# Optimization experiments

Hardware: AMD Instinct MI355X
Metric: run time of the kernel (lower is better)

Reference implementation:

```python
import jax, jax.numpy as jnp
import numpy as np

B, H, M, K = 256, 1024, 20, 20  # batch, hidden, max_ingr, pairing top_k (must be equal: M==K)
VOCAB, INGR_V = 32000, 5000


def setup_inputs() -> dict:
    key = jax.random.key(0)
    ks = jax.random.split(key, 24)
    s = 0.02
    inp = {
        "input_ids": jax.random.randint(ks[0], (1, B), 0, VOCAB),
        "hidden": jax.random.normal(ks[1], (1, B, H), jnp.float32),
        "encoder_outputs": jax.random.normal(ks[2], (M, B, 2 * H), jnp.float32),
        "input_tensor": jax.random.randint(ks[3], (B, M), 0, INGR_V),
        "pairing_ids": jax.random.randint(ks[4], (INGR_V, K), 0, INGR_V),
        # parameters
        "emb_dec": jax.random.normal(ks[5], (VOCAB, H), jnp.float32) * s,
        "enc_emb": jax.random.normal(ks[6], (INGR_V, 2 * H), jnp.float32) * s,
        "Wq_i": jax.random.normal(ks[7], (H, H), jnp.float32) * s,
        "Wk_i": jax.random.normal(ks[8], (2 * H, H), jnp.float32) * s,
        "wa_i": jax.random.normal(ks[9], (H,), jnp.float32) * s,
        "Wq_p": jax.random.normal(ks[10], (H, H), jnp.float32) * s,
        "Wk_p": jax.random.normal(ks[11], (2 * H, H), jnp.float32) * s,
        "wa_p": jax.random.normal(ks[12], (H,), jnp.float32) * s,
        "ba_p": jax.random.normal(ks[13], (), jnp.float32) * s,
        "W_lin": jax.random.normal(ks[14], (3 * H, 2 * H), jnp.float32) * s,
        "b_lin": jnp.zeros((2 * H,), jnp.float32),
        "W_ih": jax.random.normal(ks[15], (3 * H, 2 * H), jnp.float32) * s,
        "W_hh": jax.random.normal(ks[16], (3 * H, H), jnp.float32) * s,
        "b_ih": jnp.zeros((3 * H,), jnp.float32),
        "b_hh": jnp.zeros((3 * H,), jnp.float32),
        "W_out": jax.random.normal(ks[17], (H, VOCAB), jnp.float32) * s,
        "b_out": jnp.zeros((VOCAB,), jnp.float32),
    }
    return inp


def reference(input_ids, hidden, encoder_outputs, input_tensor, pairing_ids,
              emb_dec, enc_emb, Wq_i, Wk_i, wa_i, Wq_p, Wk_p, wa_p, ba_p,
              W_lin, b_lin, W_ih, W_hh, b_ih, b_hh, W_out, b_out):
    h = hidden[0]                              # (B, H)
    emb = jnp.take(emb_dec, input_ids[0], axis=0)  # (B, H)

    # ---- IngrAtt (additive attention over ingredients) ----
    # torch code does a raw .view(B, M, 2H) on a (M, B, 2H) tensor -> plain reshape
    enc = encoder_outputs.reshape(B, M, 2 * H)
    query = h @ Wq_i                           # (B, H)
    key = enc @ Wk_i                           # (B, M, H)
    scores_i = jnp.tanh(query[:, None, :] + key) @ wa_i  # (B, M)
    aw = jax.nn.softmax(scores_i, axis=-1)     # (B, M)

    # ---- retrieval: pick most-attended ingredient, gather its top-k pairings ----
    ingr_arg = jnp.argmax(aw, axis=1)                          # (B,)
    ingr_id = input_tensor[jnp.arange(B), ingr_arg]            # (B,)
    comp_ids = jnp.take(pairing_ids, ingr_id, axis=0)          # (B, K)
    comp_emb = jnp.take(enc_emb, comp_ids, axis=0)             # (B, K, 2H)

    # ---- PairingAtt ----
    q_p = h @ Wq_p                             # (B, H)
    k_p = comp_emb @ Wk_p                      # (B, K, H)
    s_p = jnp.tanh(q_p[:, None, :] + k_p) @ wa_p + ba_p  # (B, K)
    a_p = jax.nn.softmax(s_p, axis=-1)
    attn_scores = a_p * s_p                    # (B, K) softmax-weighted raw scores
    attn_app = jnp.einsum('bk,bkd->bd', attn_scores, comp_emb)  # (B, 2H)

    out_pair = jnp.concatenate([emb, attn_app], axis=-1)  # (B, 3H)
    x = out_pair @ W_lin + b_lin                           # (B, 2H) -> GRU input

    # ---- single GRU step (torch gate ordering r,z,n) ----
    gi = x @ W_ih.T + b_ih
    gh = h @ W_hh.T + b_hh
    i_r, i_z, i_n = jnp.split(gi, 3, axis=-1)
    h_r, h_z, h_n = jnp.split(gh, 3, axis=-1)
    r = jax.nn.sigmoid(i_r + h_r)
    z = jax.nn.sigmoid(i_z + h_z)
    n = jnp.tanh(i_n + r * h_n)
    h_new = (1.0 - z) * n + z * h              # (B, H)

    logits = h_new @ W_out + b_out             # (B, VOCAB)
    return logits
```

## Files before the change

### kernel.cpp

```cpp
#include <hip/hip_runtime.h>
#include <cstdio>


using f32x4   = __attribute__((ext_vector_type(4))) float;
using bf16x8  = __attribute__((ext_vector_type(8))) short;
using ushort8 = __attribute__((ext_vector_type(8))) unsigned short;

__device__ __forceinline__ unsigned short f2bf(float x) {
    unsigned u = __builtin_bit_cast(unsigned, x);
    u += 0x7fffu + ((u >> 16) & 1u);
    return (unsigned short)(u >> 16);
}
__device__ __forceinline__ float bf2f(unsigned short u) {
    return __builtin_bit_cast(float, ((unsigned)u) << 16);
}

__device__ __forceinline__ void gload16(const void* g, void* l) {
    auto gp = (const __attribute__((address_space(1))) void*)g;
    auto lp = (__attribute__((address_space(3))) void*)l;
    __builtin_amdgcn_global_load_lds(gp, lp, 16, 0, 0);
}

__device__ __forceinline__ void transpose_body(
    const float* __restrict__ in, unsigned short* __restrict__ out,
    int R, int C, int r0, int c0)
{
    __shared__ float t[32][129];
    const int tid = threadIdx.x;
    const int lr = tid >> 3;
    const int cc = (tid & 7) * 4;
    #pragma unroll
    for (int i = 0; i < 4; ++i) {
        int r = lr + 32 * i;
        float4 v = *(const float4*)(in + (size_t)(r0 + r) * C + c0 + cc);
        t[cc + 0][r] = v.x; t[cc + 1][r] = v.y;
        t[cc + 2][r] = v.z; t[cc + 3][r] = v.w;
    }
    __syncthreads();
    const int rc = (tid & 15) * 8;
    #pragma unroll
    for (int p = 0; p < 2; ++p) {
        int c = (tid >> 4) + 16 * p;
        const float* src = &t[c][rc];
        ushort8 o;
        #pragma unroll
        for (int j = 0; j < 8; ++j) o[j] = f2bf(src[j]);
        *(ushort8*)(out + (size_t)(c0 + c) * R + r0 + rc) = o;
    }
}

__global__ __launch_bounds__(256) void prep1_kernel(
    const float* __restrict__ hidden, const float* __restrict__ enc_out,
    const float* __restrict__ enc_emb,
    const float* __restrict__ Wq_i, const float* __restrict__ Wq_p,
    const float* __restrict__ Wk_i, const float* __restrict__ Wk_p,
    unsigned short* __restrict__ hb, unsigned short* __restrict__ encb,
    unsigned short* __restrict__ encembb,
    unsigned short* __restrict__ WqiT, unsigned short* __restrict__ WqpT,
    unsigned short* __restrict__ WkiT, unsigned short* __restrict__ WkpT)
{
    const int bid = blockIdx.x;
    if (bid < 20496) {
        int i = bid * 256 + threadIdx.x;
        const float* src; unsigned short* dst; int j;
        if (i < 65536)        { src = hidden;  dst = hb;      j = i; }
        else if (i < 2686976) { src = enc_out; dst = encb;    j = i - 65536; }
        else                  { src = enc_emb; dst = encembb; j = i - 2686976; }
        float4 v = ((const float4*)src)[j];
        ((ushort4*)dst)[j] = make_ushort4(f2bf(v.x), f2bf(v.y), f2bf(v.z), f2bf(v.w));
    } else if (bid < 21008) {
        int local = bid - 20496;
        int bz = local >> 8, rem = local & 255;
        transpose_body(bz ? Wq_p : Wq_i, bz ? WqpT : WqiT,
                       1024, 1024, (rem >> 5) * 128, (rem & 31) * 32);
    } else {
        int local = bid - 21008;
        int bz = local >> 9, rem = local & 511;
        transpose_body(bz ? Wk_p : Wk_i, bz ? WkpT : WkiT,
                       2048, 1024, (rem >> 5) * 128, (rem & 31) * 32);
    }
}

__global__ __launch_bounds__(256) void transpose1_kernel(
    const float* in, unsigned short* out, int R, int C)
{ transpose_body(in, out, R, C, blockIdx.y * 128, blockIdx.x * 32); }

__global__ __launch_bounds__(256) void conv2w_kernel(
    const float* __restrict__ Wih, const float* __restrict__ Whh,
    unsigned short* __restrict__ ob0, unsigned short* __restrict__ ob1)
{
    int i = blockIdx.x * 256 + threadIdx.x;
    const float* src; unsigned short* dst; int j;
    if (i < 1572864) { src = Wih; dst = ob0; j = i; }
    else             { src = Whh; dst = ob1; j = i - 1572864; }
    float4 v = ((const float4*)src)[j];
    ((ushort4*)dst)[j] = make_ushort4(f2bf(v.x), f2bf(v.y), f2bf(v.z), f2bf(v.w));
}

template<int OUTBF, bool HAS_BIAS>
__device__ __forceinline__ void gemm_core(
    const unsigned short* __restrict__ A, const unsigned short* __restrict__ Bt,
    const float* __restrict__ bias, void* __restrict__ Cout, int Ncols,
    int sA, int sB, int kLen, int m0, int n0,
    unsigned short* lA, unsigned short* lB)
{
    const int tid = threadIdx.x;
    const int lane = tid & 63, wave = tid >> 6;
    const int wr = wave >> 1, wc = wave & 1;
    const int srow = tid >> 3, schunk = tid & 7;
    const int lm = lane & 15, lk = (lane >> 4) * 8;

    f32x4 acc[4][4];
    #pragma unroll
    for (int m = 0; m < 4; ++m)
        #pragma unroll
        for (int n = 0; n < 4; ++n) { f32x4 z = {0.f,0.f,0.f,0.f}; acc[m][n] = z; }

    const unsigned short* Ag = A  + (size_t)(m0 + srow) * sA + schunk * 8;
    const unsigned short* Bg = Bt + (size_t)(n0 + srow) * sB + schunk * 8;
    const int nt = kLen >> 6;

    char* lap = (char*)lA + tid * 16;
    char* lbp = (char*)lB + tid * 16;

    for (int t = 0; t < nt; ++t) {
        #pragma unroll
        for (int i = 0; i < 4; ++i) {
            gload16(Ag + (size_t)(32 * i) * sA + t * 64, lap + i * 4096);
            gload16(Bg + (size_t)(32 * i) * sB + t * 64, lbp + i * 4096);
        }
        __syncthreads();
        #pragma unroll
        for (int kk = 0; kk < 2; ++kk) {
            bf16x8 af[4], bv[4];
            #pragma unroll
            for (int m = 0; m < 4; ++m)
                af[m] = *(const bf16x8*)((const char*)lA +
                          (wr * 64 + m * 16 + lm) * 128 + (kk * 32 + lk) * 2);
            #pragma unroll
            for (int n = 0; n < 4; ++n)
                bv[n] = *(const bf16x8*)((const char*)lB +
                          (wc * 64 + n * 16 + lm) * 128 + (kk * 32 + lk) * 2);
            #pragma unroll
            for (int m = 0; m < 4; ++m)
                #pragma unroll
                for (int n = 0; n < 4; ++n)
                    acc[m][n] = __builtin_amdgcn_mfma_f32_16x16x32_bf16(
                        af[m], bv[n], acc[m][n], 0, 0, 0);
        }
        __syncthreads();
    }

    const int rbase = m0 + wr * 64 + (lane >> 4) * 4;
    const int cbase = n0 + wc * 64 + lm;
    #pragma unroll
    for (int m = 0; m < 4; ++m) {
        #pragma unroll
        for (int n = 0; n < 4; ++n) {
            int col = cbase + n * 16;
            float bvv = HAS_BIAS ? bias[col] : 0.0f;
            #pragma unroll
            for (int j = 0; j < 4; ++j) {
                int row = rbase + m * 16 + j;
                float v = acc[m][n][j] + bvv;
                if (OUTBF)
                    ((unsigned short*)Cout)[(size_t)row * Ncols + col] = f2bf(v);
                else
                    ((float*)Cout)[(size_t)row * Ncols + col] = v;
            }
        }
    }
}

#define GEMM_SHARED \
    __shared__ unsigned short lA[8192]; __shared__ unsigned short lB[8192];

__global__ __launch_bounds__(256) void gemm_dual_kernel(
    const unsigned short* A, const unsigned short* B0, const unsigned short* B1,
    float* P0, float* P1)
{
    GEMM_SHARED
    const int g = blockIdx.z >> 2, s = blockIdx.z & 3;
    const unsigned short* Bt = (g ? B1 : B0) + s * 256;
    float* C = (g ? P1 : P0) + (size_t)s * 262144;
    gemm_core<0,false>(A + s * 256, Bt, nullptr, C, 1024, 1024, 1024, 256,
                       blockIdx.y * 128, blockIdx.x * 128, lA, lB);
}

__global__ __launch_bounds__(256) void reduceq_kernel(
    const float* __restrict__ pqQ, const float* __restrict__ pqP,
    float* __restrict__ query, float* __restrict__ qp)
{
    int i = blockIdx.x * 256 + threadIdx.x;
    const float4* p; float4* o; int j;
    if (i < 65536) { p = (const float4*)pqQ; o = (float4*)query; j = i; }
    else           { p = (const float4*)pqP; o = (float4*)qp;    j = i - 65536; }
    float4 a = p[j], b = p[j + 65536], c = p[j + 131072], d = p[j + 196608];
    o[j] = make_float4(a.x + b.x + c.x + d.x, a.y + b.y + c.y + d.y,
                       a.z + b.z + c.z + d.z, a.w + b.w + c.w + d.w);
}

__global__ __launch_bounds__(256) void gemm24_kernel(
    const unsigned short* encembb, const unsigned short* encb,
    const unsigned short* WkpT, const unsigned short* WkiT,
    unsigned short* kp_all, unsigned short* key)
{
    GEMM_SHARED
    const int z = blockIdx.z;
    const unsigned short* A  = z ? encb : encembb;
    const unsigned short* Bt = z ? WkiT : WkpT;
    unsigned short* C = z ? key : kp_all;
    gemm_core<1,false>(A, Bt, nullptr, C, 1024, 2048, 2048, 2048,
                       blockIdx.y * 128, blockIdx.x * 128, lA, lB);
}

__global__ __launch_bounds__(256) void gemm5_kernel(
    const unsigned short* A, const unsigned short* Bt, float* P)
{
    GEMM_SHARED
    const int z = blockIdx.z;
    gemm_core<0,false>(A + z * 384, Bt + z * 384, nullptr,
                       P + (size_t)z * 524288, 2048, 3072, 3072, 384,
                       blockIdx.y * 128, blockIdx.x * 128, lA, lB);
}

__global__ __launch_bounds__(256) void gemm67_kernel(
    const unsigned short* xb, const unsigned short* hb,
    const unsigned short* Wih, const unsigned short* Whh, float* pg)
{
    GEMM_SHARED
    const int g = blockIdx.z >> 2, s = blockIdx.z & 3;
    const unsigned short* A  = g ? hb  + s * 256 : xb  + s * 512;
    const unsigned short* Bt = g ? Whh + s * 256 : Wih + s * 512;
    const int sAB  = g ? 1024 : 2048;
    const int kLen = g ? 256  : 512;
    float* C = pg + (size_t)blockIdx.z * 786432;
    gemm_core<0,false>(A, Bt, nullptr, C, 3072, sAB, sAB, kLen,
                       blockIdx.y * 128, blockIdx.x * 128, lA, lB);
}

__global__ __launch_bounds__(256) void gemm8_kernel(
    const unsigned short* __restrict__ A, const float* __restrict__ Wout,
    const float* __restrict__ bias, float* __restrict__ C)
{
    __shared__ unsigned short lA0[16384]; __shared__ unsigned short lA1[16384];
    __shared__ unsigned short lB0[4096];  __shared__ unsigned short lB1[4096];
    const int tid  = threadIdx.x;
    const int lane = tid & 63, wave = tid >> 6;
    const int n0 = blockIdx.x * 64;
    const int lm = lane & 15, lk = (lane >> 4) * 8;
    const int srow = tid >> 3, schunk = tid & 7;
    const int bcol = tid & 63, bkg = tid >> 6;
    const int bsw  = (bcol & 7) << 4;

    f32x4 acc[4][4];
    #pragma unroll
    for (int m = 0; m < 4; ++m)
        #pragma unroll
        for (int n = 0; n < 4; ++n) { f32x4 z = {0.f,0.f,0.f,0.f}; acc[m][n] = z; }

    const unsigned short* Ag = A + (size_t)srow * 1024 + schunk * 8;

    auto stageA = [&](unsigned short* la_, int t) {
        char* la = (char*)la_ + tid * 16;
        #pragma unroll
        for (int i = 0; i < 8; ++i)
            gload16(Ag + (size_t)(32 * i) * 1024 + t * 64, la + i * 4096);
    };
    float bv_[16];
    auto loadB = [&](int t) {
        const float* src = Wout + (size_t)(t * 64 + bkg * 16) * 32000 + n0 + bcol;
        #pragma unroll
        for (int j = 0; j < 16; ++j) bv_[j] = src[(size_t)j * 32000];
    };
    auto writeB = [&](unsigned short* lb_) {
        ushort8 o0, o1;
        #pragma unroll
        for (int j = 0; j < 8; ++j) { o0[j] = f2bf(bv_[j]); o1[j] = f2bf(bv_[j + 8]); }
        char* base = (char*)lb_ + bcol * 128;
        *(ushort8*)(base + ((bkg * 32)      ^ bsw)) = o0;
        *(ushort8*)(base + ((bkg * 32 + 16) ^ bsw)) = o1;
    };
    auto compute = [&](const unsigned short* la_, const unsigned short* lb_) {
        #pragma unroll
        for (int kk = 0; kk < 2; ++kk) {
            bf16x8 af[4], bv[4];
            #pragma unroll
            for (int m = 0; m < 4; ++m)
                af[m] = *(const bf16x8*)((const char*)la_ +
                          (wave * 64 + m * 16 + lm) * 128 + (kk * 32 + lk) * 2);
            #pragma unroll
            for (int n = 0; n < 4; ++n) {
                int rr = n * 16 + lm;
                bv[n] = *(const bf16x8*)((const char*)lb_ +
                          rr * 128 + (((kk * 32 + lk) * 2) ^ ((rr & 7) << 4)));
            }
            #pragma unroll
            for (int m = 0; m < 4; ++m)
                #pragma unroll
                for (int n = 0; n < 4; ++n)
                    acc[m][n] = __builtin_amdgcn_mfma_f32_16x16x32_bf16(
                        af[m], bv[n], acc[m][n], 0, 0, 0);
        }
    };

    stageA(lA0, 0); loadB(0); writeB(lB0);
    __syncthreads();
    const int nt = 16;
    for (int t = 0; t < nt; t += 2) {
        if (t + 1 < nt) { stageA(lA1, t + 1); loadB(t + 1); }
        compute(lA0, lB0);
        if (t + 1 < nt) writeB(lB1);
        __syncthreads();
        if (t + 1 < nt) {
            if (t + 2 < nt) { stageA(lA0, t + 2); loadB(t + 2); }
            compute(lA1, lB1);
            if (t + 2 < nt) writeB(lB0);
            __syncthreads();
        }
    }

    const int rbase = wave * 64 + (lane >> 4) * 4;
    const int cbase = n0 + lm;
    #pragma unroll
    for (int m = 0; m < 4; ++m) {
        #pragma unroll
        for (int n = 0; n < 4; ++n) {
            int col = cbase + n * 16;
            float bvv = bias[col];
            #pragma unroll
            for (int j = 0; j < 4; ++j)
                C[(size_t)(rbase + m * 16 + j) * 32000 + col] = acc[m][n][j] + bvv;
        }
    }
}

__global__ __launch_bounds__(256) void attn_scores_kernel(
    const float* __restrict__ q, const unsigned short* __restrict__ k,
    const float* __restrict__ wa, float* __restrict__ scores)
{
    const int bm = blockIdx.x;
    const int b  = bm / 20;
    const int tid = threadIdx.x;
    float4 qv  = ((const float4*)(q + (size_t)b * 1024))[tid];
    ushort4 kv = ((const ushort4*)(k + (size_t)bm * 1024))[tid];
    float4 wv  = ((const float4*)wa)[tid];
    float p = tanhf(qv.x + bf2f(kv.x)) * wv.x + tanhf(qv.y + bf2f(kv.y)) * wv.y
            + tanhf(qv.z + bf2f(kv.z)) * wv.z + tanhf(qv.w + bf2f(kv.w)) * wv.w;
    #pragma unroll
    for (int off = 32; off > 0; off >>= 1) p += __shfl_down(p, off);
    __shared__ float sp[4];
    if ((tid & 63) == 0) sp[tid >> 6] = p;
    __syncthreads();
    if (tid == 0) scores[bm] = sp[0] + sp[1] + sp[2] + sp[3];
}

__device__ __forceinline__ int argmax_ing(
    const float* __restrict__ sc_i, const int* __restrict__ input_tensor, int b)
{
    float best = sc_i[b * 20]; int bi = 0;
    #pragma unroll
    for (int m = 1; m < 20; ++m) {
        float v = sc_i[b * 20 + m];
        if (v > best) { best = v; bi = m; }
    }
    return input_tensor[b * 20 + bi];
}

__global__ __launch_bounds__(256) void attn_scores_gather_kernel(
    const float* __restrict__ q, const unsigned short* __restrict__ kp_all,
    const float* __restrict__ wa, const float* __restrict__ ba,
    const float* __restrict__ sc_i, const int* __restrict__ input_tensor,
    const int* __restrict__ pairing_ids, float* __restrict__ scores)
{
    const int bm = blockIdx.x;
    const int b  = bm / 20;
    const int kk = bm - b * 20;
    const int tid = threadIdx.x;
    const int ing = argmax_ing(sc_i, input_tensor, b);
    const int cid = pairing_ids[ing * 20 + kk];
    float4 qv  = ((const float4*)(q + (size_t)b * 1024))[tid];
    ushort4 kv = ((const ushort4*)(kp_all + (size_t)cid * 1024))[tid];
    float4 wv  = ((const float4*)wa)[tid];
    float p = tanhf(qv.x + bf2f(kv.x)) * wv.x + tanhf(qv.y + bf2f(kv.y)) * wv.y
            + tanhf(qv.z + bf2f(kv.z)) * wv.z + tanhf(qv.w + bf2f(kv.w)) * wv.w;
    #pragma unroll
    for (int off = 32; off > 0; off >>= 1) p += __shfl_down(p, off);
    __shared__ float sp[4];
    if ((tid & 63) == 0) sp[tid >> 6] = p;
    __syncthreads();
    if (tid == 0) scores[bm] = sp[0] + sp[1] + sp[2] + sp[3] + ba[0];
}

__global__ __launch_bounds__(256) void out_pair_kernel(
    const float* __restrict__ s_p, const float* __restrict__ enc_emb,
    const float* __restrict__ sc_i, const int* __restrict__ input_tensor,
    const int* __restrict__ pairing_ids,
    const float* __restrict__ emb_dec, const int* __restrict__ input_ids,
    unsigned short* __restrict__ out_pairb)
{
    const int b = blockIdx.x / 6, seg = blockIdx.x % 6;
    const int tid = threadIdx.x;
    const int d = seg * 512 + tid * 2;
    ushort2 o;
    if (seg < 2) {
        float2 v = *(const float2*)(emb_dec + (size_t)input_ids[b] * 1024 + d);
        o.x = f2bf(v.x); o.y = f2bf(v.y);
    } else {
        const int ing = argmax_ing(sc_i, input_tensor, b);
        __shared__ float s_raw[20];
        if (tid < 20) s_raw[tid] = s_p[b * 20 + tid];
        __syncthreads();
        float mx = -1e30f;
        #pragma unroll
        for (int m = 0; m < 20; ++m) mx = fmaxf(mx, s_raw[m]);
        float den = 0.f; float w[20];
        #pragma unroll
        for (int m = 0; m < 20; ++m) { w[m] = expf(s_raw[m] - mx); den += w[m]; }
        const float inv = 1.f / den;
        const int dd = d - 1024;
        float a0 = 0.f, a1 = 0.f;
        #pragma unroll
        for (int k = 0; k < 20; ++k) {
            const int cid = pairing_ids[ing * 20 + k];
            float2 v = *(const float2*)(enc_emb + (size_t)cid * 2048 + dd);
            float a = w[k] * inv * s_raw[k];
            a0 += a * v.x; a1 += a * v.y;
        }
        o.x = f2bf(a0); o.y = f2bf(a1);
    }
    *(ushort2*)(out_pairb + (size_t)b * 3072 + d) = o;
}

__global__ __launch_bounds__(256) void reduce5_kernel(
    const float* __restrict__ P, const float* __restrict__ bias,
    unsigned short* __restrict__ xb)
{
    int i = blockIdx.x * 256 + threadIdx.x;
    const float4* p = (const float4*)P;
    float4 bb = ((const float4*)bias)[i & 511];
    float s0 = bb.x, s1 = bb.y, s2 = bb.z, s3 = bb.w;
    #pragma unroll
    for (int s = 0; s < 8; ++s) {
        float4 v = p[i + s * 131072];
        s0 += v.x; s1 += v.y; s2 += v.z; s3 += v.w;
    }
    ((ushort4*)xb)[i] = make_ushort4(f2bf(s0), f2bf(s1), f2bf(s2), f2bf(s3));
}

__global__ __launch_bounds__(256) void gru_kernel(
    const float* __restrict__ pg, const float* __restrict__ b_ih,
    const float* __restrict__ b_hh, const float* __restrict__ h,
    unsigned short* __restrict__ hnewb)
{
    int idx = blockIdx.x * 256 + threadIdx.x;
    int b = idx >> 10, j = idx & 1023;
    float ir = b_ih[j], iz = b_ih[1024 + j], in_ = b_ih[2048 + j];
    float hr = b_hh[j], hz = b_hh[1024 + j], hn  = b_hh[2048 + j];
    #pragma unroll
    for (int s = 0; s < 4; ++s) {
        const float* gi = pg + (size_t)s * 786432 + (size_t)b * 3072;
        ir  += gi[j]; iz += gi[1024 + j]; in_ += gi[2048 + j];
        const float* gh = pg + (size_t)(4 + s) * 786432 + (size_t)b * 3072;
        hr  += gh[j]; hz += gh[1024 + j]; hn  += gh[2048 + j];
    }
    float r = 1.f / (1.f + expf(-(ir + hr)));
    float z = 1.f / (1.f + expf(-(iz + hz)));
    float n = tanhf(in_ + r * hn);
    hnewb[idx] = f2bf((1.f - z) * n + z * h[idx]);
}

extern "C" void kernel_launch(void* const* d_in, const int* in_sizes, int n_in,
                              void* d_out, int out_size, void* d_ws, size_t ws_size,
                              hipStream_t stream)
{
    const int*   input_ids    = (const int*)  d_in[0];
    const float* hidden       = (const float*)d_in[1];
    const float* enc_out      = (const float*)d_in[2];
    const int*   input_tensor = (const int*)  d_in[3];
    const int*   pairing_ids  = (const int*)  d_in[4];
    const float* emb_dec      = (const float*)d_in[5];
    const float* enc_emb      = (const float*)d_in[6];
    const float* Wq_i  = (const float*)d_in[7];
    const float* Wk_i  = (const float*)d_in[8];
    const float* wa_i  = (const float*)d_in[9];
    const float* Wq_p  = (const float*)d_in[10];
    const float* Wk_p  = (const float*)d_in[11];
    const float* wa_p  = (const float*)d_in[12];
    const float* ba_p  = (const float*)d_in[13];
    const float* W_lin = (const float*)d_in[14];
    const float* b_lin = (const float*)d_in[15];
    const float* W_ih  = (const float*)d_in[16];
    const float* W_hh  = (const float*)d_in[17];
    const float* b_ih  = (const float*)d_in[18];
    const float* b_hh  = (const float*)d_in[19];
    const float* W_out = (const float*)d_in[20];
    const float* b_out = (const float*)d_in[21];

    constexpr size_t OFF_HB    = 0;
    constexpr size_t OFF_HNEW  = 524288;
    constexpr size_t OFF_WQI   = 1048576;
    constexpr size_t OFF_WQP   = 3145728;
    constexpr size_t OFF_WKI   = 5242880;
    constexpr size_t OFF_WKP   = 9437184;
    constexpr size_t OFF_ENC   = 13631488;
    constexpr size_t OFF_SLOT1 = 34603008;
    constexpr size_t OFF_SLOT2 = 55574528;
    constexpr size_t OFF_QUERY = 76546048;
    constexpr size_t OFF_QP    = 77594624;
    constexpr size_t OFF_SCI   = 78643200;
    constexpr size_t OFF_SCP   = 78667776;
    constexpr size_t OFF_PGI   = 1048576;
    constexpr size_t NEED      = 79167488;
    if (ws_size < NEED) {
        fprintf(stderr, "kernel_launch: ws_size %zu < needed %zu\n", ws_size, NEED);
        return;
    }
    char* ws = (char*)d_ws;
    unsigned short* hb     = (unsigned short*)(ws + OFF_HB);
    unsigned short* hnewb  = (unsigned short*)(ws + OFF_HNEW);
    unsigned short* WqiT   = (unsigned short*)(ws + OFF_WQI);
    unsigned short* WqpT   = (unsigned short*)(ws + OFF_WQP);
    unsigned short* WkiT   = (unsigned short*)(ws + OFF_WKI);
    unsigned short* WkpT   = (unsigned short*)(ws + OFF_WKP);
    unsigned short* encb   = (unsigned short*)(ws + OFF_ENC);
    float*          pqQ    = (float*)         (ws + OFF_SLOT1);
    float*          pqP    = (float*)         (ws + OFF_SLOT1 + 4194304);
    unsigned short* kp_all = (unsigned short*)(ws + OFF_SLOT1);
    unsigned short* key    = (unsigned short*)(ws + OFF_SLOT1 + 10485760);
    unsigned short* encembb= (unsigned short*)(ws + OFF_SLOT2);
    unsigned short* WlinT  = (unsigned short*)(ws + OFF_SLOT2);
    unsigned short* Wihb   = (unsigned short*)(ws + OFF_SLOT2);
    unsigned short* Whhb   = (unsigned short*)(ws + OFF_SLOT2 + 12582912);
    unsigned short* outp   = (unsigned short*)(ws + OFF_SLOT1);
    float*          pG5    = (float*)         (ws + OFF_SLOT1 + 1572864);
    unsigned short* xb     = (unsigned short*)(ws + OFF_SLOT1 + 18350080);
    float*          query  = (float*)         (ws + OFF_QUERY);
    float*          qp     = (float*)         (ws + OFF_QP);
    float*          sc_i   = (float*)         (ws + OFF_SCI);
    float*          sc_p   = (float*)         (ws + OFF_SCP);
    float*          pgi    = (float*)         (ws + OFF_PGI);

    prep1_kernel<<<22032, 256, 0, stream>>>(hidden, enc_out, enc_emb,
                                            Wq_i, Wq_p, Wk_i, Wk_p,
                                            hb, encb, encembb,
                                            WqiT, WqpT, WkiT, WkpT);

    gemm_dual_kernel<<<dim3(8, 2, 8), 256, 0, stream>>>(hb, WqiT, WqpT, pqQ, pqP);
    reduceq_kernel<<<512, 256, 0, stream>>>(pqQ, pqP, query, qp);

    gemm24_kernel<<<dim3(8, 40, 2), 256, 0, stream>>>(encembb, encb, WkpT, WkiT,
                                                      kp_all, key);

    attn_scores_kernel<<<5120, 256, 0, stream>>>(query, key, wa_i, sc_i);
    attn_scores_gather_kernel<<<5120, 256, 0, stream>>>(qp, kp_all, wa_p, ba_p,
                                                        sc_i, input_tensor, pairing_ids, sc_p);

    out_pair_kernel<<<1536, 256, 0, stream>>>(sc_p, enc_emb, sc_i, input_tensor,
                                              pairing_ids, emb_dec, input_ids, outp);

    transpose1_kernel<<<dim3(64, 24), 256, 0, stream>>>(W_lin, WlinT, 3072, 2048);
    gemm5_kernel<<<dim3(16, 2, 8), 256, 0, stream>>>(outp, WlinT, pG5);
    reduce5_kernel<<<512, 256, 0, stream>>>(pG5, b_lin, xb);

    conv2w_kernel<<<9216, 256, 0, stream>>>(W_ih, W_hh, Wihb, Whhb);
    gemm67_kernel<<<dim3(24, 2, 8), 256, 0, stream>>>(xb, hb, Wihb, Whhb, pgi);

    gru_kernel<<<1024, 256, 0, stream>>>(pgi, b_ih, b_hh, hidden, hnewb);

    gemm8_kernel<<<500, 256, 0, stream>>>(hnewb, W_out, b_out, (float*)d_out);
}
```

Before: 241.2 us.

## Fuse fp32-to-bf16 weight conversion into GEMMs and split-K the key projections

The standalone W_lin transpose and the W_ih/W_hh bf16 conversion kernels are removed. The GEMM kernels now read fp32 weights directly and convert them to bf16 while staging into LDS, which saves a full write and reread of the converted weights. Separately, the key-projection GEMM is split along K into two halves that store bf16 partials (one set placed in the output buffer as scratch). The attention score kernels sum the two partials. This adds launch parallelism but doubles the key reads, adds an extra bf16 rounding, and turns the W_lin B loads into strided scalar reads.

Result: faster. 230.6 us (-4.4%).

```diff
diff --git a/kernel.cpp b/kernel.cpp
--- a/kernel.cpp
+++ b/kernel.cpp
@@ -81,22 +81,6 @@
     }
 }
 
-__global__ __launch_bounds__(256) void transpose1_kernel(
-    const float* in, unsigned short* out, int R, int C)
-{ transpose_body(in, out, R, C, blockIdx.y * 128, blockIdx.x * 32); }
-
-__global__ __launch_bounds__(256) void conv2w_kernel(
-    const float* __restrict__ Wih, const float* __restrict__ Whh,
-    unsigned short* __restrict__ ob0, unsigned short* __restrict__ ob1)
-{
-    int i = blockIdx.x * 256 + threadIdx.x;
-    const float* src; unsigned short* dst; int j;
-    if (i < 1572864) { src = Wih; dst = ob0; j = i; }
-    else             { src = Whh; dst = ob1; j = i - 1572864; }
-    float4 v = ((const float4*)src)[j];
-    ((ushort4*)dst)[j] = make_ushort4(f2bf(v.x), f2bf(v.y), f2bf(v.z), f2bf(v.w));
-}
-
 template<int OUTBF, bool HAS_BIAS>
 __device__ __forceinline__ void gemm_core(
     const unsigned short* __restrict__ A, const unsigned short* __restrict__ Bt,
@@ -203,40 +187,175 @@
 __global__ __launch_bounds__(256) void gemm24_kernel(
     const unsigned short* encembb, const unsigned short* encb,
     const unsigned short* WkpT, const unsigned short* WkiT,
-    unsigned short* kp_all, unsigned short* key)
+    unsigned short* kpP, unsigned short* keyP, size_t pStride)
 {
     GEMM_SHARED
-    const int z = blockIdx.z;
-    const unsigned short* A  = z ? encb : encembb;
-    const unsigned short* Bt = z ? WkiT : WkpT;
-    unsigned short* C = z ? key : kp_all;
-    gemm_core<1,false>(A, Bt, nullptr, C, 1024, 2048, 2048, 2048,
+    const int g = blockIdx.z >> 1, h = blockIdx.z & 1;
+    const unsigned short* A  = (g ? encb : encembb) + h * 1024;
+    const unsigned short* Bt = (g ? WkiT : WkpT)    + h * 1024;
+    unsigned short* C = (g ? keyP : kpP) + (size_t)h * pStride;
+    gemm_core<1,false>(A, Bt, nullptr, C, 1024, 2048, 2048, 1024,
                        blockIdx.y * 128, blockIdx.x * 128, lA, lB);
 }
 
-__global__ __launch_bounds__(256) void gemm5_kernel(
-    const unsigned short* A, const unsigned short* Bt, float* P)
-{
-    GEMM_SHARED
-    const int z = blockIdx.z;
-    gemm_core<0,false>(A + z * 384, Bt + z * 384, nullptr,
-                       P + (size_t)z * 524288, 2048, 3072, 3072, 384,
-                       blockIdx.y * 128, blockIdx.x * 128, lA, lB);
-}
-
-__global__ __launch_bounds__(256) void gemm67_kernel(
-    const unsigned short* xb, const unsigned short* hb,
-    const unsigned short* Wih, const unsigned short* Whh, float* pg)
-{
-    GEMM_SHARED
+__global__ __launch_bounds__(256) void gemm5f_kernel(
+    const unsigned short* __restrict__ A, const float* __restrict__ Wlin,
+    float* __restrict__ P)
+{
+    __shared__ unsigned short lA[8192];
+    __shared__ unsigned short lB[8192];
+    const int tid = threadIdx.x;
+    const int lane = tid & 63, wave = tid >> 6;
+    const int wr = wave >> 1, wc = wave & 1;
+    const int m0 = blockIdx.y * 128, n0 = blockIdx.x * 128;
+    const int koff = blockIdx.z * 384;
+    const int srow = tid >> 3, schunk = tid & 7;
+    const int lm = lane & 15, lk = (lane >> 4) * 8;
+    const int bcol = tid & 127, bkg = tid >> 7;
+    const int bsw  = (bcol & 7) << 4;
+
+    f32x4 acc[4][4];
+    #pragma unroll
+    for (int m = 0; m < 4; ++m)
+        #pragma unroll
+        for (int n = 0; n < 4; ++n) { f32x4 z = {0.f,0.f,0.f,0.f}; acc[m][n] = z; }
+
+    const unsigned short* Ag = A + (size_t)(m0 + srow) * 3072 + koff + schunk * 8;
+    char* lap = (char*)lA + tid * 16;
+
+    for (int t = 0; t < 6; ++t) {
+        #pragma unroll
+        for (int i = 0; i < 4; ++i)
+            gload16(Ag + (size_t)(32 * i) * 3072 + t * 64, lap + i * 4096);
+        #pragma unroll
+        for (int hh = 0; hh < 2; ++hh) {
+            const int kbase = koff + t * 64 + bkg * 32 + hh * 16;
+            ushort8 o0, o1;
+            #pragma unroll
+            for (int j = 0; j < 8; ++j)
+                o0[j] = f2bf(Wlin[(size_t)(kbase + j) * 2048 + n0 + bcol]);
+            #pragma unroll
+            for (int j = 0; j < 8; ++j)
+                o1[j] = f2bf(Wlin[(size_t)(kbase + 8 + j) * 2048 + n0 + bcol]);
+            char* base = (char*)lB + bcol * 128;
+            *(ushort8*)(base + ((bkg * 64 + hh * 32)      ^ bsw)) = o0;
+            *(ushort8*)(base + ((bkg * 64 + hh * 32 + 16) ^ bsw)) = o1;
+        }
+        __syncthreads();
+        #pragma unroll
+        for (int kk = 0; kk < 2; ++kk) {
+            bf16x8 af[4], bv[4];
+            #pragma unroll
+            for (int m = 0; m < 4; ++m)
+                af[m] = *(const bf16x8*)((const char*)lA +
+                          (wr * 64 + m * 16 + lm) * 128 + (kk * 32 + lk) * 2);
+            #pragma unroll
+            for (int n = 0; n < 4; ++n) {
+                int rr = wc * 64 + n * 16 + lm;
+                bv[n] = *(const bf16x8*)((const char*)lB +
+                          rr * 128 + (((kk * 32 + lk) * 2) ^ ((rr & 7) << 4)));
+            }
+            #pragma unroll
+            for (int m = 0; m < 4; ++m)
+                #pragma unroll
+                for (int n = 0; n < 4; ++n)
+                    acc[m][n] = __builtin_amdgcn_mfma_f32_16x16x32_bf16(
+                        af[m], bv[n], acc[m][n], 0, 0, 0);
+        }
+        __syncthreads();
+    }
+
+    float* C = P + (size_t)blockIdx.z * 524288;
+    const int rbase = m0 + wr * 64 + (lane >> 4) * 4;
+    const int cbase = n0 + wc * 64 + lm;
+    #pragma unroll
+    for (int m = 0; m < 4; ++m)
+        #pragma unroll
+        for (int n = 0; n < 4; ++n)
+            #pragma unroll
+            for (int j = 0; j < 4; ++j)
+                C[(size_t)(rbase + m * 16 + j) * 2048 + cbase + n * 16] = acc[m][n][j];
+}
+
+__global__ __launch_bounds__(256) void gemm67f_kernel(
+    const unsigned short* __restrict__ xb, const unsigned short* __restrict__ hb,
+    const float* __restrict__ Wih, const float* __restrict__ Whh,
+    float* __restrict__ pg)
+{
+    __shared__ unsigned short lA[8192];
+    __shared__ unsigned short lB[8192];
+    const int tid = threadIdx.x;
+    const int lane = tid & 63, wave = tid >> 6;
+    const int wr = wave >> 1, wc = wave & 1;
     const int g = blockIdx.z >> 2, s = blockIdx.z & 3;
-    const unsigned short* A  = g ? hb  + s * 256 : xb  + s * 512;
-    const unsigned short* Bt = g ? Whh + s * 256 : Wih + s * 512;
-    const int sAB  = g ? 1024 : 2048;
-    const int kLen = g ? 256  : 512;
+    const unsigned short* A = g ? hb : xb;
+    const float* Bf = g ? Whh : Wih;
+    const int sA   = g ? 1024 : 2048;
+    const int koff = g ? s * 256 : s * 512;
+    const int nt   = g ? 4 : 8;
+    const int m0 = blockIdx.y * 128, n0 = blockIdx.x * 128;
+    const int srow = tid >> 3, schunk = tid & 7;
+    const int lm = lane & 15, lk = (lane >> 4) * 8;
+    const int bsw = (srow & 7) << 4;
+
+    f32x4 acc[4][4];
+    #pragma unroll
+    for (int m = 0; m < 4; ++m)
+        #pragma unroll
+        for (int n = 0; n < 4; ++n) { f32x4 z = {0.f,0.f,0.f,0.f}; acc[m][n] = z; }
+
+    const unsigned short* Ag = A  + (size_t)(m0 + srow) * sA + koff + schunk * 8;
+    const float*          Bg = Bf + (size_t)(n0 + srow) * sA + koff + schunk * 8;
+    char* lap = (char*)lA + tid * 16;
+
+    for (int t = 0; t < nt; ++t) {
+        #pragma unroll
+        for (int i = 0; i < 4; ++i)
+            gload16(Ag + (size_t)(32 * i) * sA + t * 64, lap + i * 4096);
+        #pragma unroll
+        for (int i = 0; i < 4; ++i) {
+            const float* src = Bg + (size_t)(32 * i) * sA + t * 64;
+            float4 v0 = *(const float4*)(src);
+            float4 v1 = *(const float4*)(src + 4);
+            ushort8 o;
+            o[0] = f2bf(v0.x); o[1] = f2bf(v0.y); o[2] = f2bf(v0.z); o[3] = f2bf(v0.w);
+            o[4] = f2bf(v1.x); o[5] = f2bf(v1.y); o[6] = f2bf(v1.z); o[7] = f2bf(v1.w);
+            *(ushort8*)((char*)lB + (srow + 32 * i) * 128 + ((schunk * 16) ^ bsw)) = o;
+        }
+        __syncthreads();
+        #pragma unroll
+        for (int kk = 0; kk < 2; ++kk) {
+            bf16x8 af[4], bv[4];
+            #pragma unroll
+            for (int m = 0; m < 4; ++m)
+                af[m] = *(const bf16x8*)((const char*)lA +
+                          (wr * 64 + m * 16 + lm) * 128 + (kk * 32 + lk) * 2);
+            #pragma unroll
+            for (int n = 0; n < 4; ++n) {
+                int rr = wc * 64 + n * 16 + lm;
+                bv[n] = *(const bf16x8*)((const char*)lB +
+                          rr * 128 + (((kk * 32 + lk) * 2) ^ ((rr & 7) << 4)));
+            }
+            #pragma unroll
+            for (int m = 0; m < 4; ++m)
+                #pragma unroll
+                for (int n = 0; n < 4; ++n)
+                    acc[m][n] = __builtin_amdgcn_mfma_f32_16x16x32_bf16(
+                        af[m], bv[n], acc[m][n], 0, 0, 0);
+        }
+        __syncthreads();
+    }
+
     float* C = pg + (size_t)blockIdx.z * 786432;
-    gemm_core<0,false>(A, Bt, nullptr, C, 3072, sAB, sAB, kLen,
-                       blockIdx.y * 128, blockIdx.x * 128, lA, lB);
+    const int rbase = m0 + wr * 64 + (lane >> 4) * 4;
+    const int cbase = n0 + wc * 64 + lm;
+    #pragma unroll
+    for (int m = 0; m < 4; ++m)
+        #pragma unroll
+        for (int n = 0; n < 4; ++n)
+            #pragma unroll
+            for (int j = 0; j < 4; ++j)
+                C[(size_t)(rbase + m * 16 + j) * 3072 + cbase + n * 16] = acc[m][n][j];
 }
 
 __global__ __launch_bounds__(256) void gemm8_kernel(
@@ -335,18 +454,21 @@
     }
 }
 
-__global__ __launch_bounds__(256) void attn_scores_kernel(
-    const float* __restrict__ q, const unsigned short* __restrict__ k,
-    const float* __restrict__ wa, float* __restrict__ scores)
+__global__ __launch_bounds__(256) void attn_scores2_kernel(
+    const float* __restrict__ q, const unsigned short* __restrict__ kP,
+    size_t kStride, const float* __restrict__ wa, float* __restrict__ scores)
 {
     const int bm = blockIdx.x;
     const int b  = bm / 20;
     const int tid = threadIdx.x;
     float4 qv  = ((const float4*)(q + (size_t)b * 1024))[tid];
-    ushort4 kv = ((const ushort4*)(k + (size_t)bm * 1024))[tid];
+    ushort4 k0 = ((const ushort4*)(kP + (size_t)bm * 1024))[tid];
+    ushort4 k1 = ((const ushort4*)(kP + kStride + (size_t)bm * 1024))[tid];
     float4 wv  = ((const float4*)wa)[tid];
-    float p = tanhf(qv.x + bf2f(kv.x)) * wv.x + tanhf(qv.y + bf2f(kv.y)) * wv.y
-            + tanhf(qv.z + bf2f(kv.z)) * wv.z + tanhf(qv.w + bf2f(kv.w)) * wv.w;
+    float p = tanhf(qv.x + bf2f(k0.x) + bf2f(k1.x)) * wv.x
+            + tanhf(qv.y + bf2f(k0.y) + bf2f(k1.y)) * wv.y
+            + tanhf(qv.z + bf2f(k0.z) + bf2f(k1.z)) * wv.z
+            + tanhf(qv.w + bf2f(k0.w) + bf2f(k1.w)) * wv.w;
     #pragma unroll
     for (int off = 32; off > 0; off >>= 1) p += __shfl_down(p, off);
     __shared__ float sp[4];
@@ -367,9 +489,9 @@
     return input_tensor[b * 20 + bi];
 }
 
-__global__ __launch_bounds__(256) void attn_scores_gather_kernel(
-    const float* __restrict__ q, const unsigned short* __restrict__ kp_all,
-    const float* __restrict__ wa, const float* __restrict__ ba,
+__global__ __launch_bounds__(256) void attn_scores_gather2_kernel(
+    const float* __restrict__ q, const unsigned short* __restrict__ kP,
+    size_t kStride, const float* __restrict__ wa, const float* __restrict__ ba,
     const float* __restrict__ sc_i, const int* __restrict__ input_tensor,
     const int* __restrict__ pairing_ids, float* __restrict__ scores)
 {
@@ -380,10 +502,13 @@
     const int ing = argmax_ing(sc_i, input_tensor, b);
     const int cid = pairing_ids[ing * 20 + kk];
     float4 qv  = ((const float4*)(q + (size_t)b * 1024))[tid];
-    ushort4 kv = ((const ushort4*)(kp_all + (size_t)cid * 1024))[tid];
+    ushort4 k0 = ((const ushort4*)(kP + (size_t)cid * 1024))[tid];
+    ushort4 k1 = ((const ushort4*)(kP + kStride + (size_t)cid * 1024))[tid];
     float4 wv  = ((const float4*)wa)[tid];
-    float p = tanhf(qv.x + bf2f(kv.x)) * wv.x + tanhf(qv.y + bf2f(kv.y)) * wv.y
-            + tanhf(qv.z + bf2f(kv.z)) * wv.z + tanhf(qv.w + bf2f(kv.w)) * wv.w;
+    float p = tanhf(qv.x + bf2f(k0.x) + bf2f(k1.x)) * wv.x
+            + tanhf(qv.y + bf2f(k0.y) + bf2f(k1.y)) * wv.y
+            + tanhf(qv.z + bf2f(k0.z) + bf2f(k1.z)) * wv.z
+            + tanhf(qv.w + bf2f(k0.w) + bf2f(k1.w)) * wv.w;
     #pragma unroll
     for (int off = 32; off > 0; off >>= 1) p += __shfl_down(p, off);
     __shared__ float sp[4];
@@ -526,12 +651,8 @@
     unsigned short* encb   = (unsigned short*)(ws + OFF_ENC);
     float*          pqQ    = (float*)         (ws + OFF_SLOT1);
     float*          pqP    = (float*)         (ws + OFF_SLOT1 + 4194304);
-    unsigned short* kp_all = (unsigned short*)(ws + OFF_SLOT1);
-    unsigned short* key    = (unsigned short*)(ws + OFF_SLOT1 + 10485760);
+    unsigned short* kpP    = (unsigned short*)(ws + OFF_SLOT1);
     unsigned short* encembb= (unsigned short*)(ws + OFF_SLOT2);
-    unsigned short* WlinT  = (unsigned short*)(ws + OFF_SLOT2);
-    unsigned short* Wihb   = (unsigned short*)(ws + OFF_SLOT2);
-    unsigned short* Whhb   = (unsigned short*)(ws + OFF_SLOT2 + 12582912);
     unsigned short* outp   = (unsigned short*)(ws + OFF_SLOT1);
     float*          pG5    = (float*)         (ws + OFF_SLOT1 + 1572864);
     unsigned short* xb     = (unsigned short*)(ws + OFF_SLOT1 + 18350080);
@@ -540,6 +661,9 @@
     float*          sc_i   = (float*)         (ws + OFF_SCI);
     float*          sc_p   = (float*)         (ws + OFF_SCP);
     float*          pgi    = (float*)         (ws + OFF_PGI);
+    unsigned short* keyP   = (unsigned short*)d_out;
+
+    constexpr size_t KP_STRIDE = 5120 * 1024;
 
     prep1_kernel<<<22032, 256, 0, stream>>>(hidden, enc_out, enc_emb,
                                             Wq_i, Wq_p, Wk_i, Wk_p,
@@ -549,22 +673,20 @@
     gemm_dual_kernel<<<dim3(8, 2, 8), 256, 0, stream>>>(hb, WqiT, WqpT, pqQ, pqP);
     reduceq_kernel<<<512, 256, 0, stream>>>(pqQ, pqP, query, qp);
 
-    gemm24_kernel<<<dim3(8, 40, 2), 256, 0, stream>>>(encembb, encb, WkpT, WkiT,
-                                                      kp_all, key);
-
-    attn_scores_kernel<<<5120, 256, 0, stream>>>(query, key, wa_i, sc_i);
-    attn_scores_gather_kernel<<<5120, 256, 0, stream>>>(qp, kp_all, wa_p, ba_p,
-                                                        sc_i, input_tensor, pairing_ids, sc_p);
+    gemm24_kernel<<<dim3(8, 40, 4), 256, 0, stream>>>(encembb, encb, WkpT, WkiT,
+                                                      kpP, keyP, KP_STRIDE);
+
+    attn_scores2_kernel<<<5120, 256, 0, stream>>>(query, keyP, KP_STRIDE, wa_i, sc_i);
+    attn_scores_gather2_kernel<<<5120, 256, 0, stream>>>(qp, kpP, KP_STRIDE, wa_p, ba_p,
+                                                         sc_i, input_tensor, pairing_ids, sc_p);
 
     out_pair_kernel<<<1536, 256, 0, stream>>>(sc_p, enc_emb, sc_i, input_tensor,
                                               pairing_ids, emb_dec, input_ids, outp);
 
-    transpose1_kernel<<<dim3(64, 24), 256, 0, stream>>>(W_lin, WlinT, 3072, 2048);
-    gemm5_kernel<<<dim3(16, 2, 8), 256, 0, stream>>>(outp, WlinT, pG5);
+    gemm5f_kernel<<<dim3(16, 2, 8), 256, 0, stream>>>(outp, W_lin, pG5);
     reduce5_kernel<<<512, 256, 0, stream>>>(pG5, b_lin, xb);
 
-    conv2w_kernel<<<9216, 256, 0, stream>>>(W_ih, W_hh, Wihb, Whhb);
-    gemm67_kernel<<<dim3(24, 2, 8), 256, 0, stream>>>(xb, hb, Wihb, Whhb, pgi);
+    gemm67f_kernel<<<dim3(24, 2, 8), 256, 0, stream>>>(xb, hb, W_ih, W_hh, pgi);
 
     gru_kernel<<<1024, 256, 0, stream>>>(pgi, b_ih, b_hh, hidden, hnewb);
 
```
